# Kernel tuning notes

Measured on AMD Instinct MI355X. Metric: run time of the kernel, lower is better.

Reference implementation:

```python
import jax, jax.numpy as jnp
import numpy as np

B, LQ, LK = 16, 1024, 2048
E, F, A = 512, 256, 512


def setup_inputs() -> dict:
    key = jax.random.key(0)
    ks = jax.random.split(key, 8)
    s_e = 1.0 / np.sqrt(E)
    s_f = 1.0 / np.sqrt(F)
    s_a = 1.0 / np.sqrt(A)
    return {
        "lstm_embeddings": jax.random.normal(ks[0], (B, LQ, E), jnp.float32),
        "optical_flow_features": jax.random.normal(ks[1], (B, LK, F), jnp.float32),
        "Wq": jax.random.normal(ks[2], (E, A), jnp.float32) * s_e,
        "bq": jnp.zeros((A,), jnp.float32),
        "Wk": jax.random.normal(ks[3], (F, A), jnp.float32) * s_f,
        "bk": jnp.zeros((A,), jnp.float32),
        "Wv": jax.random.normal(ks[4], (F, A), jnp.float32) * s_f,
        "bv": jnp.zeros((A,), jnp.float32),
        "Wo": jax.random.normal(ks[5], (A, E), jnp.float32) * s_a,
        "bo": jnp.zeros((E,), jnp.float32),
    }


def reference(lstm_embeddings, optical_flow_features, Wq, bq, Wk, bk, Wv, bv, Wo, bo):
    # Linear projections (x @ W + b), matching nn.Linear with W stored as [in, out]
    q = lstm_embeddings @ Wq + bq            # [B, LQ, A]
    k = optical_flow_features @ Wk + bk      # [B, LK, A]
    v = optical_flow_features @ Wv + bv      # [B, LK, A]
    # NOTE: original module does NOT scale scores by 1/sqrt(A) — stay faithful.
    scores = jnp.einsum("bqa,bka->bqk", q, k)      # [B, LQ, LK]
    weights = jax.nn.softmax(scores, axis=-1)
    context = jnp.einsum("bqk,bka->bqa", weights, v)  # [B, LQ, A]
    return context @ Wo + bo                          # [B, LQ, E]
```

## Files before the change

### kernel.cpp

```cpp
#include <hip/hip_runtime.h>


#define DEV static __device__ __forceinline__

typedef __attribute__((ext_vector_type(8))) short s8v;
typedef __attribute__((ext_vector_type(8))) _Float16 h8v;
typedef __attribute__((ext_vector_type(4))) _Float16 h4v;
typedef __attribute__((ext_vector_type(4))) float f4v;
typedef __attribute__((ext_vector_type(16))) float f16f;
typedef __attribute__((ext_vector_type(4))) float float4v;
typedef unsigned short u16;
typedef unsigned int u32;

constexpr int BB = 16;
constexpr int LQ = 1024;
constexpr int LK = 2048;
constexpr int E = 512;
constexpr int F = 256;

DEV u16 f2bf(float x) {
    u32 u = __builtin_bit_cast(u32, x);
    u += 0x7fff + ((u >> 16) & 1);
    return (u16)(u >> 16);
}
DEV float bf2f(u16 h) { return __builtin_bit_cast(float, (u32)h << 16); }

DEV f4v MF(s8v a, s8v b, f4v c) {
    return __builtin_amdgcn_mfma_f32_16x16x32_bf16(a, b, c, 0, 0, 0);
}
DEV f4v MF16(h8v a, h8v b, f4v c) {
    return __builtin_amdgcn_mfma_f32_16x16x32_f16(a, b, c, 0, 0, 0);
}
DEV f16f MF32(h8v a, h8v b, f16f c) {
    return __builtin_amdgcn_mfma_f32_32x32x16_f16(a, b, c, 0, 0, 0);
}

DEV void gll16(const _Float16* g, _Float16* l) {
    __builtin_amdgcn_global_load_lds(
        (const __attribute__((address_space(1))) u32*)g,
        (__attribute__((address_space(3))) u32*)l, 16, 0, 0);
}

__global__ __launch_bounds__(256) void prew2(
    const float* __restrict__ y, _Float16* __restrict__ yA,
    _Float16* __restrict__ yB,
    const float* __restrict__ Wq, const float* __restrict__ bq,
    const float* __restrict__ Wk, const float* __restrict__ Wv,
    const float* __restrict__ bv, const float* __restrict__ Wo,
    const float* __restrict__ bo,
    u16* __restrict__ Mhb, u16* __restrict__ Ntb,
    float* __restrict__ wvec, float* __restrict__ cvec)
{
    __shared__ __align__(16) char smem[33536];
    const int tid = threadIdx.x;
    const int bi = blockIdx.x;

    if (bi >= 67) {
        const int pb = bi - 67;
        float (*Y)[260] = (float(*)[260])smem;
        const int b = pb >> 6, t = pb & 63;
        const float* src = y + ((size_t)b * LK + t * 32) * F;
#pragma unroll
        for (int i = 0; i < 8; ++i) {
            int base = i * 1024 + tid * 4;
            int k = base >> 8, f = base & 255;
            *(float4v*)&Y[k][f] = *(const float4v*)(src + base);
        }
        __syncthreads();
        size_t tb = (size_t)(b * 64 + t) * 8192;
#pragma unroll
        for (int i = 0; i < 4; ++i) {
            int c = i * 256 + tid;
            int k = c & 31, hi = (c >> 5) & 1, fs = c >> 6;
            int f0 = fs * 16 + hi * 8;
            float4v v0 = *(const float4v*)&Y[k][f0];
            float4v v1 = *(const float4v*)&Y[k][f0 + 4];
            h8v v;
#pragma unroll
            for (int j = 0; j < 4; ++j) { v[j] = (_Float16)v0[j]; v[4 + j] = (_Float16)v1[j]; }
            *(h8v*)(yA + tb + (size_t)c * 8) = v;
        }
#pragma unroll
        for (int i = 0; i < 4; ++i) {
            int c = i * 256 + tid;
            int fl = c & 31, hi = (c >> 5) & 1, frag = c >> 6;
            int ft = frag >> 1, ks = frag & 1;
            int f = ft * 32 + fl, k0 = ks * 16 + hi * 8;
            h8v v;
#pragma unroll
            for (int j = 0; j < 8; ++j) v[j] = (_Float16)Y[k0 + j][f];
            *(h8v*)(yB + tb + (size_t)c * 8) = v;
        }
        return;
    }

    if (bi >= 64) {
        if (bi == 64) {
            const float* r = Wk + (size_t)tid * 512;
            float s = 0.f;
#pragma unroll 4
            for (int a = 0; a < 512; a += 4) {
                float4v v = *(const float4v*)(r + a);
                float4v bb = *(const float4v*)(bq + a);
                s += v[0] * bb[0] + v[1] * bb[1] + v[2] * bb[2] + v[3] * bb[3];
            }
            wvec[tid] = s;
        } else {
            int e = (bi - 65) * 256 + tid;
            float s = bo[e];
#pragma unroll 4
            for (int a = 0; a < 512; ++a) s += bv[a] * Wo[(size_t)a * 512 + e];
            cvec[e] = s;
        }
        return;
    }

    const bool ntm = bi >= 32;
    const int bj = ntm ? bi - 32 : bi;
    const int m0 = ntm ? (bj >> 2) * 64 : (bj >> 3) * 64;
    const int n0 = ntm ? (bj & 3) * 64 : (bj & 7) * 64;
    const float* Ag = ntm ? Wo : Wk;
    const float* Bg = ntm ? Wv : Wq;

    u16 (*Ash)[40] = (u16(*)[40])(smem);
    u16 (*Asl)[40] = (u16(*)[40])(smem + 5120);
    u16 (*Bsh)[40] = (u16(*)[40])(smem + 10240);
    u16 (*Bsl)[40] = (u16(*)[40])(smem + 15360);

    const int w = tid >> 6, lane = tid & 63;
    const int g = lane >> 4, qn = lane & 15;
    const int wr = w & 1, wc = w >> 1;

    f4v acc[2][2];
#pragma unroll
    for (int i = 0; i < 2; ++i)
#pragma unroll
        for (int j = 0; j < 2; ++j) acc[i][j] = (f4v){0.f, 0.f, 0.f, 0.f};

    for (int k0 = 0; k0 < 512; k0 += 32) {
        __syncthreads();
        if (!ntm) {
            int r = tid & 63, c = (tid >> 6) * 8;
            const float* s = Ag + (size_t)(m0 + r) * 512 + k0 + c;
            float4v v0 = *(const float4v*)s, v1 = *(const float4v*)(s + 4);
            short hh[8], ll[8];
#pragma unroll
            for (int i = 0; i < 8; ++i) {
                float x = (i < 4) ? v0[i] : v1[i - 4];
                u16 h = f2bf(x);
                hh[i] = (short)h;
                ll[i] = (short)f2bf(x - bf2f(h));
            }
            *(s8v*)&Ash[r][c] = (s8v){hh[0],hh[1],hh[2],hh[3],hh[4],hh[5],hh[6],hh[7]};
            *(s8v*)&Asl[r][c] = (s8v){ll[0],ll[1],ll[2],ll[3],ll[4],ll[5],ll[6],ll[7]};
        } else {
            int k = tid >> 3, mc = (tid & 7) * 8;
            const float* s = Ag + (size_t)(k0 + k) * 512 + m0 + mc;
            float4v v0 = *(const float4v*)s, v1 = *(const float4v*)(s + 4);
#pragma unroll
            for (int i = 0; i < 8; ++i) {
                float x = (i < 4) ? v0[i] : v1[i - 4];
                u16 h = f2bf(x);
                Ash[mc + i][k] = h;
                Asl[mc + i][k] = f2bf(x - bf2f(h));
            }
        }
        {
            int r = tid & 63, c = (tid >> 6) * 8;
            const float* s = Bg + (size_t)(n0 + r) * 512 + k0 + c;
            float4v v0 = *(const float4v*)s, v1 = *(const float4v*)(s + 4);
            short hh[8], ll[8];
#pragma unroll
            for (int i = 0; i < 8; ++i) {
                float x = (i < 4) ? v0[i] : v1[i - 4];
                u16 h = f2bf(x);
                hh[i] = (short)h;
                ll[i] = (short)f2bf(x - bf2f(h));
            }
            *(s8v*)&Bsh[r][c] = (s8v){hh[0],hh[1],hh[2],hh[3],hh[4],hh[5],hh[6],hh[7]};
            *(s8v*)&Bsl[r][c] = (s8v){ll[0],ll[1],ll[2],ll[3],ll[4],ll[5],ll[6],ll[7]};
        }
        __syncthreads();

        s8v ah[2], al[2], bh[2], bl[2];
#pragma unroll
        for (int mt = 0; mt < 2; ++mt) {
            ah[mt] = *(const s8v*)&Ash[wr * 32 + mt * 16 + qn][g * 8];
            al[mt] = *(const s8v*)&Asl[wr * 32 + mt * 16 + qn][g * 8];
        }
#pragma unroll
        for (int nt = 0; nt < 2; ++nt) {
            bh[nt] = *(const s8v*)&Bsh[wc * 32 + nt * 16 + qn][g * 8];
            bl[nt] = *(const s8v*)&Bsl[wc * 32 + nt * 16 + qn][g * 8];
        }
#pragma unroll
        for (int mt = 0; mt < 2; ++mt)
#pragma unroll
            for (int nt = 0; nt < 2; ++nt) {
                acc[mt][nt] = MF(ah[mt], bh[nt], acc[mt][nt]);
                acc[mt][nt] = MF(ah[mt], bl[nt], acc[mt][nt]);
                acc[mt][nt] = MF(al[mt], bh[nt], acc[mt][nt]);
            }
    }

#pragma unroll
    for (int mt = 0; mt < 2; ++mt)
#pragma unroll
        for (int nt = 0; nt < 2; ++nt)
#pragma unroll
            for (int r = 0; r < 4; ++r) {
                int gm = m0 + wr * 32 + mt * 16 + 4 * g + r;
                int gn = n0 + wc * 32 + nt * 16 + qn;
                float v = acc[mt][nt][r];
                if (!ntm) {
                    size_t off = (size_t)((gn >> 5) * 16 + (gm >> 4)) * 512 +
                                 (gm & 15) * 8 + ((gn >> 3) & 3) * 128 + (gn & 7);
                    Mhb[off] = __builtin_bit_cast(u16, (_Float16)v);
                } else {
                    size_t off = (size_t)((gn >> 5) * 32 + (gm >> 4)) * 512 +
                                 (gm & 15) * 8 + ((gn >> 3) & 3) * 128 + (gn & 7);
                    Ntb[off] = __builtin_bit_cast(u16, (_Float16)v);
                }
            }
}

__global__ __launch_bounds__(256) void qprime7(
    const float* __restrict__ x, const u16* __restrict__ Mhb,
    const float* __restrict__ wv, _Float16* __restrict__ q16)
{
    __shared__ _Float16 Xs[2][64][40];
    const int tid = threadIdx.x, w = tid >> 6, lane = tid & 63;
    const int g = lane >> 4, qn = lane & 15;
    const int id = blockIdx.x;
    const int logical = (id & 7) * 64 + (id >> 3);
    const int m0 = (logical >> 1) * 64;
    const int nh = (logical & 1) * 8;
    const int srow = tid >> 2, scol = (tid & 3) * 8;
    const _Float16* Mh = (const _Float16*)Mhb;

    f4v acc[8];
#pragma unroll
    for (int n = 0; n < 8; ++n) acc[n] = (f4v){0.f, 0.f, 0.f, 0.f};

    float4v a0, a1;
    auto LDA = [&](int k0) {
        const float* s = x + (size_t)(m0 + srow) * 512 + k0 + scol;
        a0 = *(const float4v*)s;
        a1 = *(const float4v*)(s + 4);
    };
    auto STA = [&](int buf) {
        h8v v;
#pragma unroll
        for (int j = 0; j < 4; ++j) { v[j] = (_Float16)a0[j]; v[4 + j] = (_Float16)a1[j]; }
        *(h8v*)&Xs[buf][srow][scol] = v;
    };
    h8v b0[8], b1[8];
    auto LDB0 = [&](int t) {
        const int fb = t * 16 + nh;
#pragma unroll
        for (int nt = 0; nt < 8; ++nt)
            b0[nt] = *(const h8v*)(Mh + (size_t)(fb + nt) * 512 + lane * 8);
    };
    auto LDB1 = [&](int t) {
        const int fb = t * 16 + nh;
#pragma unroll
        for (int nt = 0; nt < 8; ++nt)
            b1[nt] = *(const h8v*)(Mh + (size_t)(fb + nt) * 512 + lane * 8);
    };

    LDA(0); STA(0); LDA(32); LDB0(0);
    __syncthreads();

#pragma unroll
    for (int t = 0; t < 16; ++t) {
        const int cur = t & 1;
        if (t < 15) { if (cur == 0) LDB1(t + 1); else LDB0(t + 1); }
        h8v af = *(const h8v*)&Xs[cur][w * 16 + qn][g * 8];
        if (cur == 0) {
#pragma unroll
            for (int nt = 0; nt < 8; ++nt) acc[nt] = MF16(af, b0[nt], acc[nt]);
        } else {
#pragma unroll
            for (int nt = 0; nt < 8; ++nt) acc[nt] = MF16(af, b1[nt], acc[nt]);
        }
        if (t < 15) {
            STA(cur ^ 1);
            if (t < 14) LDA((t + 2) * 32);
            __syncthreads();
        }
    }

#pragma unroll
    for (int nt = 0; nt < 8; ++nt) {
        int col = (nh + nt) * 16 + qn;
        float wvc = wv[col];
#pragma unroll
        for (int r = 0; r < 4; ++r) {
            int row = m0 + w * 16 + 4 * g + r;
            q16[(size_t)row * 256 + col] = (_Float16)(acc[nt][r] + wvc);
        }
    }
}

__global__ __launch_bounds__(512) void flash9s(
    const _Float16* __restrict__ q16, const _Float16* __restrict__ yA,
    const _Float16* __restrict__ yB, _Float16* __restrict__ part,
    float* __restrict__ ml)
{
    __shared__ _Float16 Asb[2][2][8192];
    __shared__ _Float16 Bsb[2][2][8192];
    __shared__ _Float16 Pls[8][1024];

    const int tid = threadIdx.x;
    const int w = tid >> 6, lane = tid & 63;
    const int q32 = lane & 31, hi = lane >> 5;

    int id = blockIdx.x;
    int xcd = id & 7, slot = id >> 3;
    int grp = xcd + 8 * (slot >> 2);
    int qb = slot & 3;
    int b = grp >> 2, z = grp & 3;
    const int qw = qb * 256 + w * 32;

    h8v qf[16];
    {
        const _Float16* qp = q16 + ((size_t)b * LQ + qw + q32) * 256 + hi * 8;
#pragma unroll
        for (int s = 0; s < 16; ++s) qf[s] = *(const h8v*)(qp + s * 16);
    }
    f16f ctx[8];
#pragma unroll
    for (int i = 0; i < 8; ++i) ctx[i] = (f16f){};
    float mrun = -3.0e38f, lrun = 0.f;

    const size_t tbe = (size_t)(b * 64 + z * 16) * 8192;

    auto STAGE = [&](int sup, int buf) {
#pragma unroll
        for (int j = 0; j < 2; ++j) {
            const _Float16* ga = yA + tbe + (size_t)(sup * 2 + j) * 8192 + tid * 8;
            const _Float16* gb = yB + tbe + (size_t)(sup * 2 + j) * 8192 + tid * 8;
            gll16(ga,        &Asb[buf][j][tid * 8]);
            gll16(ga + 4096, &Asb[buf][j][tid * 8 + 4096]);
            gll16(gb,        &Bsb[buf][j][tid * 8]);
            gll16(gb + 4096, &Bsb[buf][j][tid * 8 + 4096]);
        }
    };

    STAGE(0, 0);
    __syncthreads();

    int buf = 0;
    for (int s = 0; s < 8; ++s) {
        if (s < 7) STAGE(s + 1, buf ^ 1);
#pragma unroll
        for (int j = 0; j < 2; ++j) {
            const _Float16* Ap = &Asb[buf][j][0];
            const _Float16* Bp = &Bsb[buf][j][0];
            f16f S = (f16f){};
            __builtin_amdgcn_s_setprio(1);
#pragma unroll
            for (int fs = 0; fs < 16; ++fs) {
                h8v a = *(const h8v*)(Ap + fs * 512 + lane * 8);
                S = MF32(a, qf[fs], S);
            }
            __builtin_amdgcn_s_setprio(0);
            float mt = S[0];
#pragma unroll
            for (int r = 1; r < 16; ++r) mt = fmaxf(mt, S[r]);
            mt = fmaxf(mt, __shfl_xor(mt, 32));
            if (!__all(mt <= mrun + 8.f)) {
                float mnew = fmaxf(mrun, mt);
                float alpha = __expf(mrun - mnew);
                lrun *= alpha;
#pragma unroll
                for (int r = 0; r < 16; ++r) {
                    int qr = (r & 3) + 8 * (r >> 2) + 4 * hi;
                    float ar = __shfl(alpha, qr);
#pragma unroll
                    for (int ft = 0; ft < 8; ++ft) ctx[ft][r] *= ar;
                }
                mrun = mnew;
            }
            float p[16], ps = 0.f;
#pragma unroll
            for (int r = 0; r < 16; ++r) { p[r] = __expf(S[r] - mrun); ps += p[r]; }
            ps += __shfl_xor(ps, 32);
            lrun += ps;
            {
                _Float16* pw = &Pls[w][0];
#pragma unroll
                for (int r2 = 0; r2 < 4; ++r2) {
                    h4v pk = (h4v){(_Float16)p[4 * r2], (_Float16)p[4 * r2 + 1],
                                   (_Float16)p[4 * r2 + 2], (_Float16)p[4 * r2 + 3]};
                    *(h4v*)(pw + (r2 >> 1) * 512 + (r2 & 1) * 256 + q32 * 8 + hi * 4) = pk;
                }
            }
            __builtin_amdgcn_s_setprio(1);
#pragma unroll
            for (int ks = 0; ks < 2; ++ks) {
                h8v pa = *(const h8v*)(&Pls[w][ks * 512] + lane * 8);
#pragma unroll
                for (int ft = 0; ft < 8; ++ft) {
                    h8v bf = *(const h8v*)(Bp + (ft * 2 + ks) * 512 + lane * 8);
                    ctx[ft] = MF32(pa, bf, ctx[ft]);
                }
            }
            __builtin_amdgcn_s_setprio(0);
        }
        __syncthreads();
        buf ^= 1;
    }

    float linv = 1.f / lrun;
    _Float16* pp = part + ((size_t)z * (BB * LQ) + (size_t)b * LQ + qw) * 256;
#pragma unroll
    for (int r = 0; r < 16; ++r) {
        int qr = (r & 3) + 8 * (r >> 2) + 4 * hi;
        float ir = __shfl(linv, qr);
#pragma unroll
        for (int ft = 0; ft < 8; ++ft)
            pp[(size_t)qr * 256 + ft * 32 + q32] = (_Float16)(ctx[ft][r] * ir);
    }
    if (hi == 0) {
        size_t mi = (size_t)z * (BB * LQ) + (size_t)b * LQ + qw + q32;
        ml[2 * mi + 0] = mrun;
        ml[2 * mi + 1] = lrun;
    }
}

__global__ __launch_bounds__(256) void gemm2c2(
    const _Float16* __restrict__ part, const float* __restrict__ ml,
    const u16* __restrict__ Ntb, const float* __restrict__ cvec,
    float* __restrict__ out)
{
    __shared__ _Float16 Asb[32][40];
    __shared__ float scl[32][4];
    const int tid = threadIdx.x;
    const int w = tid >> 6, lane = tid & 63;
    const int g = lane >> 4, qn = lane & 15;
    const int m0 = blockIdx.x * 32;
    constexpr size_t PL = (size_t)BB * LQ * F;
    constexpr size_t PR = (size_t)BB * LQ;

    if (tid < 32) {
        size_t i = m0 + tid;
        float m0v = ml[2 * i], l0v = ml[2 * i + 1];
        float m1v = ml[2 * (PR + i)], l1v = ml[2 * (PR + i) + 1];
        float m2v = ml[2 * (2 * PR + i)], l2v = ml[2 * (2 * PR + i) + 1];
        float m3v = ml[2 * (3 * PR + i)], l3v = ml[2 * (3 * PR + i) + 1];
        float M = fmaxf(fmaxf(m0v, m1v), fmaxf(m2v, m3v));
        float e0v = __expf(m0v - M), e1v = __expf(m1v - M);
        float e2v = __expf(m2v - M), e3v = __expf(m3v - M);
        float inv = 1.f / (l0v * e0v + l1v * e1v + l2v * e2v + l3v * e3v);
        scl[tid][0] = l0v * e0v * inv;
        scl[tid][1] = l1v * e1v * inv;
        scl[tid][2] = l2v * e2v * inv;
        scl[tid][3] = l3v * e3v * inv;
    }

    f4v acc[2][8];
#pragma unroll
    for (int i = 0; i < 2; ++i)
#pragma unroll
        for (int j = 0; j < 8; ++j) acc[i][j] = (f4v){0.f, 0.f, 0.f, 0.f};

    for (int k0 = 0; k0 < F; k0 += 32) {
        __syncthreads();
        {
            int r = tid >> 3, cc = (tid & 7) * 4;
            size_t base = (size_t)(m0 + r) * F + k0 + cc;
            h4v p0 = *(const h4v*)(part + base);
            h4v p1 = *(const h4v*)(part + PL + base);
            h4v p2 = *(const h4v*)(part + 2 * PL + base);
            h4v p3 = *(const h4v*)(part + 3 * PL + base);
            float s0 = scl[r][0], s1 = scl[r][1], s2 = scl[r][2], s3 = scl[r][3];
#pragma unroll
            for (int i = 0; i < 4; ++i) {
                float v = (float)p0[i] * s0 + (float)p1[i] * s1 +
                          (float)p2[i] * s2 + (float)p3[i] * s3;
                Asb[r][cc + i] = (_Float16)v;
            }
        }
        __syncthreads();

        h8v ah[2];
#pragma unroll
        for (int mt = 0; mt < 2; ++mt)
            ah[mt] = *(const h8v*)&Asb[mt * 16 + qn][g * 8];
#pragma unroll
        for (int nt = 0; nt < 8; ++nt) {
            h8v bh = *(const h8v*)((const _Float16*)Ntb +
                     (size_t)((k0 >> 5) * 32 + w * 8 + nt) * 512 + lane * 8);
            acc[0][nt] = MF16(ah[0], bh, acc[0][nt]);
            acc[1][nt] = MF16(ah[1], bh, acc[1][nt]);
        }
    }

#pragma unroll
    for (int mt = 0; mt < 2; ++mt)
#pragma unroll
        for (int nt = 0; nt < 8; ++nt)
#pragma unroll
            for (int r = 0; r < 4; ++r) {
                int gm = m0 + mt * 16 + 4 * g + r;
                int gn = w * 128 + nt * 16 + qn;
                out[(size_t)gm * E + gn] = acc[mt][nt][r] + cvec[gn];
            }
}

extern "C" void kernel_launch(void* const* d_in, const int* in_sizes, int n_in,
                              void* d_out, int out_size, void* d_ws, size_t ws_size,
                              hipStream_t stream)
{
    const float* x  = (const float*)d_in[0];
    const float* y  = (const float*)d_in[1];
    const float* Wq = (const float*)d_in[2];
    const float* bq = (const float*)d_in[3];
    const float* Wk = (const float*)d_in[4];
    const float* Wv = (const float*)d_in[6];
    const float* bv = (const float*)d_in[7];
    const float* Wo = (const float*)d_in[8];
    const float* bo = (const float*)d_in[9];
    float* out = (float*)d_out;

    char* ws = (char*)d_ws;
    size_t off = 0;
    auto alloc = [&](size_t bytes) -> char* {
        char* p = ws + off;
        off = (off + bytes + 255) & ~(size_t)255;
        return p;
    };
    u16* Mhb  = (u16*)alloc(sizeof(u16) * F * E);
    float* wvec = (float*)alloc(sizeof(float) * F);
    float* cvec = (float*)alloc(sizeof(float) * E);
    u16* Ntb  = (u16*)alloc(sizeof(u16) * E * F);
    _Float16* q16 = (_Float16*)alloc(sizeof(u16) * (size_t)BB * LQ * F);
    _Float16* yA  = (_Float16*)alloc(sizeof(u16) * (size_t)BB * LK * F);
    _Float16* yB  = (_Float16*)alloc(sizeof(u16) * (size_t)BB * LK * F);
    _Float16* part = (_Float16*)alloc(sizeof(u16) * 4 * (size_t)BB * LQ * F);
    float* ml = (float*)alloc(sizeof(float) * 2 * 4 * (size_t)BB * LQ);
    (void)ws_size; (void)in_sizes; (void)n_in; (void)out_size;

    prew2<<<dim3(1091), dim3(256), 0, stream>>>(
        y, yA, yB, Wq, bq, Wk, Wv, bv, Wo, bo, Mhb, Ntb, wvec, cvec);
    qprime7<<<dim3(512), dim3(256), 0, stream>>>(x, Mhb, wvec, q16);
    flash9s<<<dim3(256), dim3(512), 0, stream>>>(q16, yA, yB, part, ml);
    gemm2c2<<<dim3(BB * LQ / 32), dim3(256), 0, stream>>>(
        part, ml, Ntb, cvec, out);
}
```

Measured before the change: 130.9 us.

## Fuse q-projection, flash attention and output GEMM into one cooperative kernel

Merges the three post-prep kernels (q projection, split-K flash attention, combine plus output projection) into a single cooperative launch of 256 blocks of 512 threads, using grid.sync between phases and one shared-memory buffer reused by all three. The aim is to remove two kernel launch gaps and their tail drain. In exchange, the q-projection and output GEMM phases now run on only 256 blocks with larger per-block tiles (64 rows each) instead of 512 blocks, which lowers parallelism in those phases. Grid-wide barriers also add their own cost.

```diff
diff --git a/kernel.cpp b/kernel.cpp
--- a/kernel.cpp
+++ b/kernel.cpp
@@ -1,5 +1,8 @@
 #include <hip/hip_runtime.h>
-
+#include <hip/hip_cooperative_groups.h>
+
+
+namespace cg = cooperative_groups;
 
 #define DEV static __device__ __forceinline__
 
@@ -224,289 +227,287 @@
             }
 }
 
-__global__ __launch_bounds__(256) void qprime7(
+__global__ __launch_bounds__(512) void fused(
     const float* __restrict__ x, const u16* __restrict__ Mhb,
-    const float* __restrict__ wv, _Float16* __restrict__ q16)
-{
-    __shared__ _Float16 Xs[2][64][40];
-    const int tid = threadIdx.x, w = tid >> 6, lane = tid & 63;
-    const int g = lane >> 4, qn = lane & 15;
-    const int id = blockIdx.x;
-    const int logical = (id & 7) * 64 + (id >> 3);
-    const int m0 = (logical >> 1) * 64;
-    const int nh = (logical & 1) * 8;
-    const int srow = tid >> 2, scol = (tid & 3) * 8;
-    const _Float16* Mh = (const _Float16*)Mhb;
-
-    f4v acc[8];
-#pragma unroll
-    for (int n = 0; n < 8; ++n) acc[n] = (f4v){0.f, 0.f, 0.f, 0.f};
-
-    float4v a0, a1;
-    auto LDA = [&](int k0) {
-        const float* s = x + (size_t)(m0 + srow) * 512 + k0 + scol;
-        a0 = *(const float4v*)s;
-        a1 = *(const float4v*)(s + 4);
-    };
-    auto STA = [&](int buf) {
-        h8v v;
-#pragma unroll
-        for (int j = 0; j < 4; ++j) { v[j] = (_Float16)a0[j]; v[4 + j] = (_Float16)a1[j]; }
-        *(h8v*)&Xs[buf][srow][scol] = v;
-    };
-    h8v b0[8], b1[8];
-    auto LDB0 = [&](int t) {
-        const int fb = t * 16 + nh;
-#pragma unroll
-        for (int nt = 0; nt < 8; ++nt)
-            b0[nt] = *(const h8v*)(Mh + (size_t)(fb + nt) * 512 + lane * 8);
-    };
-    auto LDB1 = [&](int t) {
-        const int fb = t * 16 + nh;
-#pragma unroll
-        for (int nt = 0; nt < 8; ++nt)
-            b1[nt] = *(const h8v*)(Mh + (size_t)(fb + nt) * 512 + lane * 8);
-    };
-
-    LDA(0); STA(0); LDA(32); LDB0(0);
-    __syncthreads();
-
-#pragma unroll
-    for (int t = 0; t < 16; ++t) {
-        const int cur = t & 1;
-        if (t < 15) { if (cur == 0) LDB1(t + 1); else LDB0(t + 1); }
-        h8v af = *(const h8v*)&Xs[cur][w * 16 + qn][g * 8];
-        if (cur == 0) {
-#pragma unroll
-            for (int nt = 0; nt < 8; ++nt) acc[nt] = MF16(af, b0[nt], acc[nt]);
-        } else {
-#pragma unroll
-            for (int nt = 0; nt < 8; ++nt) acc[nt] = MF16(af, b1[nt], acc[nt]);
-        }
-        if (t < 15) {
-            STA(cur ^ 1);
-            if (t < 14) LDA((t + 2) * 32);
-            __syncthreads();
-        }
-    }
-
-#pragma unroll
-    for (int nt = 0; nt < 8; ++nt) {
-        int col = (nh + nt) * 16 + qn;
-        float wvc = wv[col];
-#pragma unroll
-        for (int r = 0; r < 4; ++r) {
-            int row = m0 + w * 16 + 4 * g + r;
-            q16[(size_t)row * 256 + col] = (_Float16)(acc[nt][r] + wvc);
-        }
-    }
-}
-
-__global__ __launch_bounds__(512) void flash9s(
-    const _Float16* __restrict__ q16, const _Float16* __restrict__ yA,
-    const _Float16* __restrict__ yB, _Float16* __restrict__ part,
-    float* __restrict__ ml)
-{
-    __shared__ _Float16 Asb[2][2][8192];
-    __shared__ _Float16 Bsb[2][2][8192];
-    __shared__ _Float16 Pls[8][1024];
-
-    const int tid = threadIdx.x;
-    const int w = tid >> 6, lane = tid & 63;
-    const int q32 = lane & 31, hi = lane >> 5;
-
-    int id = blockIdx.x;
-    int xcd = id & 7, slot = id >> 3;
-    int grp = xcd + 8 * (slot >> 2);
-    int qb = slot & 3;
-    int b = grp >> 2, z = grp & 3;
-    const int qw = qb * 256 + w * 32;
-
-    h8v qf[16];
-    {
-        const _Float16* qp = q16 + ((size_t)b * LQ + qw + q32) * 256 + hi * 8;
-#pragma unroll
-        for (int s = 0; s < 16; ++s) qf[s] = *(const h8v*)(qp + s * 16);
-    }
-    f16f ctx[8];
-#pragma unroll
-    for (int i = 0; i < 8; ++i) ctx[i] = (f16f){};
-    float mrun = -3.0e38f, lrun = 0.f;
-
-    const size_t tbe = (size_t)(b * 64 + z * 16) * 8192;
-
-    auto STAGE = [&](int sup, int buf) {
-#pragma unroll
-        for (int j = 0; j < 2; ++j) {
-            const _Float16* ga = yA + tbe + (size_t)(sup * 2 + j) * 8192 + tid * 8;
-            const _Float16* gb = yB + tbe + (size_t)(sup * 2 + j) * 8192 + tid * 8;
-            gll16(ga,        &Asb[buf][j][tid * 8]);
-            gll16(ga + 4096, &Asb[buf][j][tid * 8 + 4096]);
-            gll16(gb,        &Bsb[buf][j][tid * 8]);
-            gll16(gb + 4096, &Bsb[buf][j][tid * 8 + 4096]);
-        }
-    };
-
-    STAGE(0, 0);
-    __syncthreads();
-
-    int buf = 0;
-    for (int s = 0; s < 8; ++s) {
-        if (s < 7) STAGE(s + 1, buf ^ 1);
-#pragma unroll
-        for (int j = 0; j < 2; ++j) {
-            const _Float16* Ap = &Asb[buf][j][0];
-            const _Float16* Bp = &Bsb[buf][j][0];
-            f16f S = (f16f){};
-            __builtin_amdgcn_s_setprio(1);
-#pragma unroll
-            for (int fs = 0; fs < 16; ++fs) {
-                h8v a = *(const h8v*)(Ap + fs * 512 + lane * 8);
-                S = MF32(a, qf[fs], S);
-            }
-            __builtin_amdgcn_s_setprio(0);
-            float mt = S[0];
-#pragma unroll
-            for (int r = 1; r < 16; ++r) mt = fmaxf(mt, S[r]);
-            mt = fmaxf(mt, __shfl_xor(mt, 32));
-            if (!__all(mt <= mrun + 8.f)) {
-                float mnew = fmaxf(mrun, mt);
-                float alpha = __expf(mrun - mnew);
-                lrun *= alpha;
-#pragma unroll
-                for (int r = 0; r < 16; ++r) {
-                    int qr = (r & 3) + 8 * (r >> 2) + 4 * hi;
-                    float ar = __shfl(alpha, qr);
-#pragma unroll
-                    for (int ft = 0; ft < 8; ++ft) ctx[ft][r] *= ar;
-                }
-                mrun = mnew;
-            }
-            float p[16], ps = 0.f;
-#pragma unroll
-            for (int r = 0; r < 16; ++r) { p[r] = __expf(S[r] - mrun); ps += p[r]; }
-            ps += __shfl_xor(ps, 32);
-            lrun += ps;
-            {
-                _Float16* pw = &Pls[w][0];
-#pragma unroll
-                for (int r2 = 0; r2 < 4; ++r2) {
-                    h4v pk = (h4v){(_Float16)p[4 * r2], (_Float16)p[4 * r2 + 1],
-                                   (_Float16)p[4 * r2 + 2], (_Float16)p[4 * r2 + 3]};
-                    *(h4v*)(pw + (r2 >> 1) * 512 + (r2 & 1) * 256 + q32 * 8 + hi * 4) = pk;
-                }
-            }
-            __builtin_amdgcn_s_setprio(1);
-#pragma unroll
-            for (int ks = 0; ks < 2; ++ks) {
-                h8v pa = *(const h8v*)(&Pls[w][ks * 512] + lane * 8);
-#pragma unroll
-                for (int ft = 0; ft < 8; ++ft) {
-                    h8v bf = *(const h8v*)(Bp + (ft * 2 + ks) * 512 + lane * 8);
-                    ctx[ft] = MF32(pa, bf, ctx[ft]);
-                }
-            }
-            __builtin_amdgcn_s_setprio(0);
-        }
-        __syncthreads();
-        buf ^= 1;
-    }
-
-    float linv = 1.f / lrun;
-    _Float16* pp = part + ((size_t)z * (BB * LQ) + (size_t)b * LQ + qw) * 256;
-#pragma unroll
-    for (int r = 0; r < 16; ++r) {
-        int qr = (r & 3) + 8 * (r >> 2) + 4 * hi;
-        float ir = __shfl(linv, qr);
-#pragma unroll
-        for (int ft = 0; ft < 8; ++ft)
-            pp[(size_t)qr * 256 + ft * 32 + q32] = (_Float16)(ctx[ft][r] * ir);
-    }
-    if (hi == 0) {
-        size_t mi = (size_t)z * (BB * LQ) + (size_t)b * LQ + qw + q32;
-        ml[2 * mi + 0] = mrun;
-        ml[2 * mi + 1] = lrun;
-    }
-}
-
-__global__ __launch_bounds__(256) void gemm2c2(
-    const _Float16* __restrict__ part, const float* __restrict__ ml,
+    const float* __restrict__ wv, _Float16* __restrict__ q16,
+    const _Float16* __restrict__ yA, const _Float16* __restrict__ yB,
+    _Float16* __restrict__ part, float* __restrict__ ml,
     const u16* __restrict__ Ntb, const float* __restrict__ cvec,
     float* __restrict__ out)
 {
-    __shared__ _Float16 Asb[32][40];
-    __shared__ float scl[32][4];
+    __shared__ __align__(16) char smem[147456];
+    cg::grid_group grid = cg::this_grid();
+
     const int tid = threadIdx.x;
     const int w = tid >> 6, lane = tid & 63;
     const int g = lane >> 4, qn = lane & 15;
-    const int m0 = blockIdx.x * 32;
+    const int bi = blockIdx.x;
     constexpr size_t PL = (size_t)BB * LQ * F;
     constexpr size_t PR = (size_t)BB * LQ;
 
-    if (tid < 32) {
-        size_t i = m0 + tid;
-        float m0v = ml[2 * i], l0v = ml[2 * i + 1];
-        float m1v = ml[2 * (PR + i)], l1v = ml[2 * (PR + i) + 1];
-        float m2v = ml[2 * (2 * PR + i)], l2v = ml[2 * (2 * PR + i) + 1];
-        float m3v = ml[2 * (3 * PR + i)], l3v = ml[2 * (3 * PR + i) + 1];
-        float M = fmaxf(fmaxf(m0v, m1v), fmaxf(m2v, m3v));
-        float e0v = __expf(m0v - M), e1v = __expf(m1v - M);
-        float e2v = __expf(m2v - M), e3v = __expf(m3v - M);
-        float inv = 1.f / (l0v * e0v + l1v * e1v + l2v * e2v + l3v * e3v);
-        scl[tid][0] = l0v * e0v * inv;
-        scl[tid][1] = l1v * e1v * inv;
-        scl[tid][2] = l2v * e2v * inv;
-        scl[tid][3] = l3v * e3v * inv;
+    {
+        _Float16 (*Xs)[64][40] = (_Float16(*)[64][40])smem;
+        const int w4 = w & 3;
+        const int nh = (w >> 2) * 8;
+        const int m0 = bi * 64;
+        const int srow = tid >> 3, scol = (tid & 7) * 4;
+        const _Float16* Mh = (const _Float16*)Mhb;
+
+        f4v acc[8];
+#pragma unroll
+        for (int n = 0; n < 8; ++n) acc[n] = (f4v){0.f, 0.f, 0.f, 0.f};
+
+        float4v a0;
+        auto LDA = [&](int k0) {
+            a0 = *(const float4v*)(x + (size_t)(m0 + srow) * 512 + k0 + scol);
+        };
+        auto STA = [&](int buf) {
+            h4v v = (h4v){(_Float16)a0[0], (_Float16)a0[1],
+                          (_Float16)a0[2], (_Float16)a0[3]};
+            *(h4v*)&Xs[buf][srow][scol] = v;
+        };
+        h8v b0[8], b1[8];
+        auto LDB0 = [&](int t) {
+            const int fb = t * 16 + nh;
+#pragma unroll
+            for (int nt = 0; nt < 8; ++nt)
+                b0[nt] = *(const h8v*)(Mh + (size_t)(fb + nt) * 512 + lane * 8);
+        };
+        auto LDB1 = [&](int t) {
+            const int fb = t * 16 + nh;
+#pragma unroll
+            for (int nt = 0; nt < 8; ++nt)
+                b1[nt] = *(const h8v*)(Mh + (size_t)(fb + nt) * 512 + lane * 8);
+        };
+
+        LDA(0); STA(0); LDA(32); LDB0(0);
+        __syncthreads();
+
+#pragma unroll
+        for (int t = 0; t < 16; ++t) {
+            const int cur = t & 1;
+            if (t < 15) { if (cur == 0) LDB1(t + 1); else LDB0(t + 1); }
+            h8v af = *(const h8v*)&Xs[cur][w4 * 16 + qn][g * 8];
+            if (cur == 0) {
+#pragma unroll
+                for (int nt = 0; nt < 8; ++nt) acc[nt] = MF16(af, b0[nt], acc[nt]);
+            } else {
+#pragma unroll
+                for (int nt = 0; nt < 8; ++nt) acc[nt] = MF16(af, b1[nt], acc[nt]);
+            }
+            if (t < 15) {
+                STA(cur ^ 1);
+                if (t < 14) LDA((t + 2) * 32);
+                __syncthreads();
+            }
+        }
+
+#pragma unroll
+        for (int nt = 0; nt < 8; ++nt) {
+            int col = (nh + nt) * 16 + qn;
+            float wvc = wv[col];
+#pragma unroll
+            for (int r = 0; r < 4; ++r) {
+                int row = m0 + w4 * 16 + 4 * g + r;
+                q16[(size_t)row * 256 + col] = (_Float16)(acc[nt][r] + wvc);
+            }
+        }
     }
 
-    f4v acc[2][8];
-#pragma unroll
-    for (int i = 0; i < 2; ++i)
-#pragma unroll
-        for (int j = 0; j < 8; ++j) acc[i][j] = (f4v){0.f, 0.f, 0.f, 0.f};
-
-    for (int k0 = 0; k0 < F; k0 += 32) {
+    grid.sync();
+
+    {
+        _Float16 (*Asb)[2][8192] = (_Float16(*)[2][8192])smem;
+        _Float16 (*Bsb)[2][8192] = (_Float16(*)[2][8192])(smem + 65536);
+        _Float16 (*Pls)[1024]    = (_Float16(*)[1024])(smem + 131072);
+
+        const int q32 = lane & 31, hi = lane >> 5;
+        int xcd = bi & 7, slot = bi >> 3;
+        int grp = xcd + 8 * (slot >> 2);
+        int qb = slot & 3;
+        int b = grp >> 2, z = grp & 3;
+        const int qw = qb * 256 + w * 32;
+
+        h8v qf[16];
+        {
+            const _Float16* qp = q16 + ((size_t)b * LQ + qw + q32) * 256 + hi * 8;
+#pragma unroll
+            for (int s = 0; s < 16; ++s) qf[s] = *(const h8v*)(qp + s * 16);
+        }
+        f16f ctx[8];
+#pragma unroll
+        for (int i = 0; i < 8; ++i) ctx[i] = (f16f){};
+        float mrun = -3.0e38f, lrun = 0.f;
+
+        const size_t tbe = (size_t)(b * 64 + z * 16) * 8192;
+
+        auto STAGE = [&](int sup, int buf) {
+#pragma unroll
+            for (int j = 0; j < 2; ++j) {
+                const _Float16* ga = yA + tbe + (size_t)(sup * 2 + j) * 8192 + tid * 8;
+                const _Float16* gb = yB + tbe + (size_t)(sup * 2 + j) * 8192 + tid * 8;
+                gll16(ga,        &Asb[buf][j][tid * 8]);
+                gll16(ga + 4096, &Asb[buf][j][tid * 8 + 4096]);
+                gll16(gb,        &Bsb[buf][j][tid * 8]);
+                gll16(gb + 4096, &Bsb[buf][j][tid * 8 + 4096]);
+            }
+        };
+
+        STAGE(0, 0);
         __syncthreads();
-        {
-            int r = tid >> 3, cc = (tid & 7) * 4;
-            size_t base = (size_t)(m0 + r) * F + k0 + cc;
-            h4v p0 = *(const h4v*)(part + base);
-            h4v p1 = *(const h4v*)(part + PL + base);
-            h4v p2 = *(const h4v*)(part + 2 * PL + base);
-            h4v p3 = *(const h4v*)(part + 3 * PL + base);
-            float s0 = scl[r][0], s1 = scl[r][1], s2 = scl[r][2], s3 = scl[r][3];
-#pragma unroll
-            for (int i = 0; i < 4; ++i) {
-                float v = (float)p0[i] * s0 + (float)p1[i] * s1 +
-                          (float)p2[i] * s2 + (float)p3[i] * s3;
-                Asb[r][cc + i] = (_Float16)v;
-            }
-        }
-        __syncthreads();
-
-        h8v ah[2];
+
+        int buf = 0;
+        for (int s = 0; s < 8; ++s) {
+            if (s < 7) STAGE(s + 1, buf ^ 1);
+#pragma unroll
+            for (int j = 0; j < 2; ++j) {
+                const _Float16* Ap = &Asb[buf][j][0];
+                const _Float16* Bp = &Bsb[buf][j][0];
+                f16f S = (f16f){};
+                __builtin_amdgcn_s_setprio(1);
+#pragma unroll
+                for (int fs = 0; fs < 16; ++fs) {
+                    h8v a = *(const h8v*)(Ap + fs * 512 + lane * 8);
+                    S = MF32(a, qf[fs], S);
+                }
+                __builtin_amdgcn_s_setprio(0);
+                float mt = S[0];
+#pragma unroll
+                for (int r = 1; r < 16; ++r) mt = fmaxf(mt, S[r]);
+                mt = fmaxf(mt, __shfl_xor(mt, 32));
+                if (!__all(mt <= mrun + 8.f)) {
+                    float mnew = fmaxf(mrun, mt);
+                    float alpha = __expf(mrun - mnew);
+                    lrun *= alpha;
+#pragma unroll
+                    for (int r = 0; r < 16; ++r) {
+                        int qr = (r & 3) + 8 * (r >> 2) + 4 * hi;
+                        float ar = __shfl(alpha, qr);
+#pragma unroll
+                        for (int ft = 0; ft < 8; ++ft) ctx[ft][r] *= ar;
+                    }
+                    mrun = mnew;
+                }
+                float p[16], ps = 0.f;
+#pragma unroll
+                for (int r = 0; r < 16; ++r) { p[r] = __expf(S[r] - mrun); ps += p[r]; }
+                ps += __shfl_xor(ps, 32);
+                lrun += ps;
+                {
+                    _Float16* pw = &Pls[w][0];
+#pragma unroll
+                    for (int r2 = 0; r2 < 4; ++r2) {
+                        h4v pk = (h4v){(_Float16)p[4 * r2], (_Float16)p[4 * r2 + 1],
+                                       (_Float16)p[4 * r2 + 2], (_Float16)p[4 * r2 + 3]};
+                        *(h4v*)(pw + (r2 >> 1) * 512 + (r2 & 1) * 256 + q32 * 8 + hi * 4) = pk;
+                    }
+                }
+                __builtin_amdgcn_s_setprio(1);
+#pragma unroll
+                for (int ks = 0; ks < 2; ++ks) {
+                    h8v pa = *(const h8v*)(&Pls[w][ks * 512] + lane * 8);
+#pragma unroll
+                    for (int ft = 0; ft < 8; ++ft) {
+                        h8v bf = *(const h8v*)(Bp + (ft * 2 + ks) * 512 + lane * 8);
+                        ctx[ft] = MF32(pa, bf, ctx[ft]);
+                    }
+                }
+                __builtin_amdgcn_s_setprio(0);
+            }
+            __syncthreads();
+            buf ^= 1;
+        }
+
+        float linv = 1.f / lrun;
+        _Float16* pp = part + ((size_t)z * PR + (size_t)b * LQ + qw) * 256;
+#pragma unroll
+        for (int r = 0; r < 16; ++r) {
+            int qr = (r & 3) + 8 * (r >> 2) + 4 * hi;
+            float ir = __shfl(linv, qr);
+#pragma unroll
+            for (int ft = 0; ft < 8; ++ft)
+                pp[(size_t)qr * 256 + ft * 32 + q32] = (_Float16)(ctx[ft][r] * ir);
+        }
+        if (hi == 0) {
+            size_t mi = (size_t)z * PR + (size_t)b * LQ + qw + q32;
+            ml[2 * mi + 0] = mrun;
+            ml[2 * mi + 1] = lrun;
+        }
+    }
+
+    grid.sync();
+
+    {
+        _Float16 (*Asb2)[40] = (_Float16(*)[40])smem;
+        float (*scl)[4] = (float(*)[4])(smem + 8192);
+        const int m0 = bi * 64;
+        const int wr = w >> 2, wc = w & 3;
+
+        if (tid < 64) {
+            size_t i = m0 + tid;
+            float m0v = ml[2 * i], l0v = ml[2 * i + 1];
+            float m1v = ml[2 * (PR + i)], l1v = ml[2 * (PR + i) + 1];
+            float m2v = ml[2 * (2 * PR + i)], l2v = ml[2 * (2 * PR + i) + 1];
+            float m3v = ml[2 * (3 * PR + i)], l3v = ml[2 * (3 * PR + i) + 1];
+            float M = fmaxf(fmaxf(m0v, m1v), fmaxf(m2v, m3v));
+            float e0v = __expf(m0v - M), e1v = __expf(m1v - M);
+            float e2v = __expf(m2v - M), e3v = __expf(m3v - M);
+            float inv = 1.f / (l0v * e0v + l1v * e1v + l2v * e2v + l3v * e3v);
+            scl[tid][0] = l0v * e0v * inv;
+            scl[tid][1] = l1v * e1v * inv;
+            scl[tid][2] = l2v * e2v * inv;
+            scl[tid][3] = l3v * e3v * inv;
+        }
+
+        f4v acc[2][8];
+#pragma unroll
+        for (int i = 0; i < 2; ++i)
+#pragma unroll
+            for (int j = 0; j < 8; ++j) acc[i][j] = (f4v){0.f, 0.f, 0.f, 0.f};
+
+        for (int k0 = 0; k0 < F; k0 += 32) {
+            __syncthreads();
+            {
+                int r = tid >> 3, cc = (tid & 7) * 4;
+                size_t base = (size_t)(m0 + r) * F + k0 + cc;
+                h4v p0 = *(const h4v*)(part + base);
+                h4v p1 = *(const h4v*)(part + PL + base);
+                h4v p2 = *(const h4v*)(part + 2 * PL + base);
+                h4v p3 = *(const h4v*)(part + 3 * PL + base);
+                float s0 = scl[r][0], s1 = scl[r][1], s2 = scl[r][2], s3 = scl[r][3];
+#pragma unroll
+                for (int i = 0; i < 4; ++i) {
+                    float v = (float)p0[i] * s0 + (float)p1[i] * s1 +
+                              (float)p2[i] * s2 + (float)p3[i] * s3;
+                    Asb2[r][cc + i] = (_Float16)v;
+                }
+            }
+            __syncthreads();
+
+            h8v ah[2];
+#pragma unroll
+            for (int mt = 0; mt < 2; ++mt)
+                ah[mt] = *(const h8v*)&Asb2[wr * 32 + mt * 16 + qn][g * 8];
+#pragma unroll
+            for (int nt = 0; nt < 8; ++nt) {
+                h8v bh = *(const h8v*)((const _Float16*)Ntb +
+                         (size_t)((k0 >> 5) * 32 + wc * 8 + nt) * 512 + lane * 8);
+                acc[0][nt] = MF16(ah[0], bh, acc[0][nt]);
+                acc[1][nt] = MF16(ah[1], bh, acc[1][nt]);
+            }
+        }
+
 #pragma unroll
         for (int mt = 0; mt < 2; ++mt)
-            ah[mt] = *(const h8v*)&Asb[mt * 16 + qn][g * 8];
-#pragma unroll
-        for (int nt = 0; nt < 8; ++nt) {
-            h8v bh = *(const h8v*)((const _Float16*)Ntb +
-                     (size_t)((k0 >> 5) * 32 + w * 8 + nt) * 512 + lane * 8);
-            acc[0][nt] = MF16(ah[0], bh, acc[0][nt]);
-            acc[1][nt] = MF16(ah[1], bh, acc[1][nt]);
-        }
+#pragma unroll
+            for (int nt = 0; nt < 8; ++nt)
+#pragma unroll
+                for (int r = 0; r < 4; ++r) {
+                    int gm = m0 + wr * 32 + mt * 16 + 4 * g + r;
+                    int gn = wc * 128 + nt * 16 + qn;
+                    out[(size_t)gm * E + gn] = acc[mt][nt][r] + cvec[gn];
+                }
     }
-
-#pragma unroll
-    for (int mt = 0; mt < 2; ++mt)
-#pragma unroll
-        for (int nt = 0; nt < 8; ++nt)
-#pragma unroll
-            for (int r = 0; r < 4; ++r) {
-                int gm = m0 + mt * 16 + 4 * g + r;
-                int gn = w * 128 + nt * 16 + qn;
-                out[(size_t)gm * E + gn] = acc[mt][nt][r] + cvec[gn];
-            }
 }
 
 extern "C" void kernel_launch(void* const* d_in, const int* in_sizes, int n_in,
@@ -544,8 +545,10 @@
 
     prew2<<<dim3(1091), dim3(256), 0, stream>>>(
         y, yA, yB, Wq, bq, Wk, Wv, bv, Wo, bo, Mhb, Ntb, wvec, cvec);
-    qprime7<<<dim3(512), dim3(256), 0, stream>>>(x, Mhb, wvec, q16);
-    flash9s<<<dim3(256), dim3(512), 0, stream>>>(q16, yA, yB, part, ml);
-    gemm2c2<<<dim3(BB * LQ / 32), dim3(256), 0, stream>>>(
-        part, ml, Ntb, cvec, out);
-}
+
+    void* kargs[] = {(void*)&x, (void*)&Mhb, (void*)&wvec, (void*)&q16,
+                     (void*)&yA, (void*)&yB, (void*)&part, (void*)&ml,
+                     (void*)&Ntb, (void*)&cvec, (void*)&out};
+    hipLaunchCooperativeKernel((void*)fused, dim3(256), dim3(512),
+                               kargs, 0, stream);
+}
```

After: 208.3 us. +59.1%, slower.
